# Kernel tuning notes

Hardware: AMD Instinct MI355X
Metric: run time of the kernel (lower is better)

The kernel has to match this reference:

```python
import jax, jax.numpy as jnp
import numpy as np

B, N, DIM, HID, MAXN = 2048, 65536, 256, 512, 64
MID_KEY = (MAXN + HID) // 2   # 288
MID_VAL = (DIM + HID) // 2    # 384
MID_DEC = (HID + DIM) // 2    # 384
MID_SZ  = (HID + 1) // 2      # 256

def _ln(x, g, b):
    m = x.mean(-1, keepdims=True)
    v = ((x - m) ** 2).mean(-1, keepdims=True)
    return (x - m) * jax.lax.rsqrt(v + 1e-5) * g + b

def _mish(x):
    return x * jnp.tanh(jax.nn.softplus(x))

def _mlp_ln(x, W1, b1, g, be, W2, b2):
    return _mish(_ln(x @ W1 + b1, g, be)) @ W2 + b2

def _mlp(x, W1, b1, W2, b2):
    return _mish(x @ W1 + b1) @ W2 + b2

def setup_inputs():
    key = jax.random.key(0)
    ks = iter(jax.random.split(key, 40))
    def rn(shape, s=0.05):
        return jax.random.normal(next(ks), shape, jnp.float32) * s
    x = jax.random.normal(next(ks), (N, DIM), jnp.float32)
    batch = jnp.sort(jax.random.randint(next(ks), (N,), 0, B)).astype(jnp.int32)
    z32 = lambda *s: jnp.zeros(s, jnp.float32)
    o32 = lambda *s: jnp.ones(s, jnp.float32)
    return dict(
        x=x, batch=batch, n_batches=B,
        e_rank_W=rn((DIM, 1)), e_rank_b=z32(1),
        e_card_W=rn((1, HID)), e_card_b=z32(HID),
        e_key_W1=rn((MAXN, MID_KEY)), e_key_b1=z32(MID_KEY), e_key_g=o32(MID_KEY), e_key_be=z32(MID_KEY),
        e_key_W2=rn((MID_KEY, HID)), e_key_b2=z32(HID),
        e_val_W1=rn((DIM, MID_VAL)), e_val_b1=z32(MID_VAL), e_val_g=o32(MID_VAL), e_val_be=z32(MID_VAL),
        e_val_W2=rn((MID_VAL, HID)), e_val_b2=z32(HID),
        d_key_W1=rn((MAXN, MID_KEY)), d_key_b1=z32(MID_KEY), d_key_g=o32(MID_KEY), d_key_be=z32(MID_KEY),
        d_key_W2=rn((MID_KEY, HID)), d_key_b2=z32(HID),
        d_dec_W1=rn((HID, MID_DEC)), d_dec_b1=z32(MID_DEC),
        d_dec_W2=rn((MID_DEC, DIM)), d_dec_b2=z32(DIM),
        d_size_W1=rn((HID, MID_SZ)), d_size_b1=z32(MID_SZ), d_size_g=o32(MID_SZ), d_size_be=z32(MID_SZ),
        d_size_W2=rn((MID_SZ, 1)), d_size_b2=z32(1),
    )

def reference(x, batch, n_batches, e_rank_W, e_rank_b, e_card_W, e_card_b,
              e_key_W1, e_key_b1, e_key_g, e_key_be, e_key_W2, e_key_b2,
              e_val_W1, e_val_b1, e_val_g, e_val_be, e_val_W2, e_val_b2,
              d_key_W1, d_key_b1, d_key_g, d_key_be, d_key_W2, d_key_b2,
              d_dec_W1, d_dec_b1, d_dec_W2, d_dec_b2,
              d_size_W1, d_size_b1, d_size_g, d_size_be, d_size_W2, d_size_b2):
    max_n = e_key_W1.shape[0]
    n_pts = x.shape[0]
    # ---- Encoder ----
    n = jax.ops.segment_sum(jnp.ones(n_pts, jnp.float32), batch, num_segments=n_batches).astype(jnp.int32)
    mag = jnp.abs(x @ e_rank_W + e_rank_b)[:, 0]                 # [N]
    sort_key = batch.astype(jnp.float32) * jnp.max(mag) + mag    # sort within each set by |rank|
    idx = jnp.argsort(sort_key)
    xs = x[idx]
    starts = jnp.cumsum(n) - n                                   # per-set offsets (batch is sorted)
    pos_idx = jnp.arange(n_pts) - starts[batch]                  # rank within each set
    pos = jax.nn.one_hot(pos_idx, max_n, dtype=x.dtype)
    y = _mlp_ln(xs, e_val_W1, e_val_b1, e_val_g, e_val_be, e_val_W2, e_val_b2) \
      * _mlp_ln(pos, e_key_W1, e_key_b1, e_key_g, e_key_be, e_key_W2, e_key_b2)
    z = jax.ops.segment_sum(y, batch, num_segments=n_batches) \
      + n.astype(jnp.float32)[:, None] @ e_card_W + e_card_b     # [B, HID]
    # ---- Decoder ----
    n_logits = _mlp_ln(z, d_size_W1, d_size_b1, d_size_g, d_size_be, d_size_W2, d_size_b2)  # [B, 1]
    n_dec = jnp.clip(jnp.round(n_logits[:, 0]), 0, max_n).astype(jnp.int32)
    keys = _mlp_ln(jnp.eye(max_n, dtype=x.dtype),                # onehot positions 0..max_n-1
                   d_key_W1, d_key_b1, d_key_g, d_key_be, d_key_W2, d_key_b2)  # [max_n, HID]
    zp = z[:, None, :] * keys[None, :, :]                        # [B, max_n, HID] (repeat_interleave -> dense+mask)
    xf = _mlp(zp, d_dec_W1, d_dec_b1, d_dec_W2, d_dec_b2)        # [B, max_n, DIM]
    mask = jnp.arange(max_n)[None, :] < n_dec[:, None]           # valid rows per set
    x_out = (xf * mask[..., None].astype(xf.dtype)).reshape(-1, xf.shape[-1])
    batch_out = jnp.repeat(jnp.arange(n_batches, dtype=jnp.int32), max_n)
    return x_out, batch_out, mask.reshape(-1)
```

## Files before the change

### kernel.cpp

```cpp
#include <hip/hip_runtime.h>

#define NPTS   65536
#define NB     2048
#define DIMX   256
#define HIDN   512
#define MAXNN  64
#define MIDK   288
#define MIDV   384
#define MIDD   384
#define MIDS   256

typedef unsigned short ushort_t;
typedef __attribute__((ext_vector_type(8))) short short8;
typedef __attribute__((ext_vector_type(4))) float f32x4;

__device__ __forceinline__ float mishf(float x) {
    float e = __expf(fminf(x, 30.f));
    float n = e * (e + 2.f);
    return x * n * __builtin_amdgcn_rcpf(n + 2.f);
}
__device__ __forceinline__ ushort_t f2bf(float f) {
    unsigned u = __float_as_uint(f);
    u += 0x7fffu + ((u >> 16) & 1u);
    return (ushort_t)(u >> 16);
}
__device__ __forceinline__ float bf2f(ushort_t h) {
    return __uint_as_float(((unsigned)h) << 16);
}
__device__ __forceinline__ void dma16(const void* g, void* lds) {
    __builtin_amdgcn_global_load_lds(
        (const __attribute__((address_space(1))) unsigned int*)g,
        (__attribute__((address_space(3))) unsigned int*)lds, 16, 0, 0);
}
__device__ __forceinline__ int lbound(const int* __restrict__ a, int lo, int hi, int v) {
    while (lo < hi) { int m = (lo + hi) >> 1; if (a[m] < v) lo = m + 1; else hi = m; }
    return lo;
}

#define SETUP_TBL   129
#define SETUP_Z     (SETUP_TBL + NB)
#define SETUP_WT    (SETUP_Z + 144)
#define SETUP_TOTAL (SETUP_WT + 2048)

__global__ __launch_bounds__(512)
void k_setup(const float* __restrict__ eW1, const float* __restrict__ eb1,
             const float* __restrict__ eg, const float* __restrict__ ebe,
             const float* __restrict__ eW2, const float* __restrict__ eb2,
             const float* __restrict__ dW1, const float* __restrict__ db1,
             const float* __restrict__ dg, const float* __restrict__ dbe,
             const float* __restrict__ dW2, const float* __restrict__ db2,
             float* __restrict__ enc_tbl, float* __restrict__ dec_tbl,
             const int* __restrict__ batch, const float* __restrict__ cardW,
             const float* __restrict__ cardb, float* __restrict__ z,
             const float* __restrict__ V0, ushort_t* __restrict__ T0,
             const float* __restrict__ V1, ushort_t* __restrict__ T1,
             const float* __restrict__ V2, ushort_t* __restrict__ T2,
             const float* __restrict__ V3, ushort_t* __restrict__ T3,
             const float* __restrict__ x, const float* __restrict__ rW,
             const float* __restrict__ rb, float* __restrict__ mag,
             float* __restrict__ blockmax, ushort_t* __restrict__ xb)
{
    const int blk = blockIdx.x;
    const int t = threadIdx.x;
    if (blk < SETUP_TBL) {
        const float *W1, *b1, *g, *be, *W2, *b2; float* out; int wrow;
        if (blk < 65) {
            W1 = eW1; b1 = eb1; g = eg; be = ebe; W2 = eW2; b2 = eb2;
            out = enc_tbl + blk * HIDN; wrow = (blk < 64) ? blk : -1;
        } else {
            int r = blk - 65;
            W1 = dW1; b1 = db1; g = dg; be = dbe; W2 = dW2; b2 = db2;
            out = dec_tbl + r * HIDN; wrow = r;
        }
        __shared__ float h[MIDK];
        __shared__ float red[512];
        float v = 0.f;
        if (t < MIDK) v = b1[t] + (wrow >= 0 ? W1[wrow * MIDK + t] : 0.f);
        red[t] = (t < MIDK) ? v : 0.f;
        __syncthreads();
        for (int o = 256; o > 0; o >>= 1) { if (t < o) red[t] += red[t + o]; __syncthreads(); }
        float m = red[0] / (float)MIDK;
        __syncthreads();
        float d = v - m;
        red[t] = (t < MIDK) ? d * d : 0.f;
        __syncthreads();
        for (int o = 256; o > 0; o >>= 1) { if (t < o) red[t] += red[t + o]; __syncthreads(); }
        float rs = rsqrtf(red[0] / (float)MIDK + 1e-5f);
        __syncthreads();
        if (t < MIDK) h[t] = mishf(d * rs * g[t] + be[t]);
        __syncthreads();
        float acc = b2[t];
        #pragma unroll 8
        for (int k = 0; k < MIDK; ++k) acc = fmaf(h[k], W2[k * HIDN + t], acc);
        out[t] = acc;
    } else if (blk < SETUP_Z) {
        int b = blk - SETUP_TBL;
        int s = lbound(batch, 0, NPTS, b);
        int e = lbound(batch, s, NPTS, b + 1);
        float n = (float)(e - s);
        z[b * HIDN + t] = fmaf(n, cardW[t], cardb[t]);
    } else if (blk < SETUP_WT) {
        int tile = blk - SETUP_Z;
        const float* W; ushort_t* T; int K, N;
        if (tile < 24)       { W = V0; T = T0; K = 256; N = 384; }
        else if (tile < 72)  { tile -= 24;  W = V1; T = T1; K = 384; N = 512; }
        else if (tile < 120) { tile -= 72;  W = V2; T = T2; K = 512; N = 384; }
        else                 { tile -= 120; W = V3; T = T3; K = 384; N = 256; }
        int ntn = N >> 6;
        int k0 = (tile / ntn) * 64, n0 = (tile % ntn) * 64;
        __shared__ float lds[64][65];
        #pragma unroll
        for (int pass = 0; pass < 8; ++pass) {
            int kk = pass * 8 + (t >> 6);
            lds[kk][t & 63] = W[(size_t)(k0 + kk) * N + n0 + (t & 63)];
        }
        __syncthreads();
        #pragma unroll
        for (int pass = 0; pass < 8; ++pass) {
            int nn = pass * 8 + (t >> 6);
            T[(size_t)(n0 + nn) * K + k0 + (t & 63)] = f2bf(lds[t & 63][nn]);
        }
    } else {
        int mw = blk - SETUP_WT;
        const int lane = t & 63;
        const int w = t >> 6;
        int gw = mw * 8 + w;
        float4 wv = *(const float4*)(rW + lane * 4);
        float bias = rb[0];
        float lmax = 0.f;
        for (int pt = gw; pt < NPTS; pt += 16384) {
            float4 xv = *(const float4*)(x + (size_t)pt * DIMX + lane * 4);
            ushort4 u;
            u.x = f2bf(xv.x); u.y = f2bf(xv.y); u.z = f2bf(xv.z); u.w = f2bf(xv.w);
            *(ushort4*)(xb + (size_t)pt * DIMX + lane * 4) = u;
            double d = (double)xv.x * wv.x + (double)xv.y * wv.y
                     + (double)xv.z * wv.z + (double)xv.w * wv.w;
            #pragma unroll
            for (int o = 32; o > 0; o >>= 1) d += __shfl_xor(d, o);
            float s = fabsf((float)(d + (double)bias));
            if (lane == 0) mag[pt] = s;
            lmax = fmaxf(lmax, s);
        }
        __shared__ float wm8[8];
        if (lane == 0) wm8[w] = lmax;
        __syncthreads();
        if (t == 0) {
            float m = wm8[0];
            #pragma unroll
            for (int i = 1; i < 8; ++i) m = fmaxf(m, wm8[i]);
            blockmax[mw] = m;
        }
    }
}

__global__ __launch_bounds__(256)
void k_rank(const int* __restrict__ batch, const float* __restrict__ mag,
            const float* __restrict__ blockmax, int* __restrict__ kidx)
{
    __shared__ float red[256];
    const int t = threadIdx.x;
    float m = 0.f;
    for (int i = t; i < 2048; i += 256) m = fmaxf(m, blockmax[i]);
    red[t] = m;
    __syncthreads();
    for (int o = 128; o > 0; o >>= 1) { if (t < o) red[t] = fmaxf(red[t], red[t + o]); __syncthreads(); }
    float M = red[0];

    int i = blockIdx.x * 256 + t;
    if (i >= NPTS) return;
    int b = batch[i];
    int s = lbound(batch, 0, NPTS, b);
    int e = lbound(batch, s, NPTS, b + 1);
    float kb = __fmul_rn((float)b, M);
    float ki = __fadd_rn(kb, mag[i]);
    int r = 0;
    for (int j = s; j < e; ++j) {
        float kj = __fadd_rn(kb, mag[j]);
        r += (kj < ki) || (kj == ki && j < i);
    }
    kidx[i] = (r < MAXNN) ? r : MAXNN;
}

__global__ __launch_bounds__(256)
void k_size(const float* __restrict__ z, const float* __restrict__ W1,
            const float* __restrict__ b1, const float* __restrict__ g,
            const float* __restrict__ be, const float* __restrict__ W2,
            const float* __restrict__ b2, int* __restrict__ ndec)
{
    const int b0 = blockIdx.x * 4, t = threadIdx.x;
    __shared__ float zr[4][HIDN];
    __shared__ float red[4][256];
    #pragma unroll
    for (int gI = 0; gI < 4; ++gI) {
        zr[gI][t] = z[(b0 + gI) * HIDN + t];
        zr[gI][t + 256] = z[(b0 + gI) * HIDN + 256 + t];
    }
    __syncthreads();
    float acc[4];
    float bb1 = b1[t];
    #pragma unroll
    for (int gI = 0; gI < 4; ++gI) acc[gI] = bb1;
    #pragma unroll 8
    for (int k = 0; k < HIDN; ++k) {
        float wv = W1[k * MIDS + t];
        #pragma unroll
        for (int gI = 0; gI < 4; ++gI) acc[gI] = fmaf(zr[gI][k], wv, acc[gI]);
    }
    #pragma unroll
    for (int gI = 0; gI < 4; ++gI) red[gI][t] = acc[gI];
    __syncthreads();
    for (int o = 128; o > 0; o >>= 1) {
        if (t < o) {
            #pragma unroll
            for (int gI = 0; gI < 4; ++gI) red[gI][t] += red[gI][t + o];
        }
        __syncthreads();
    }
    float mm[4];
    #pragma unroll
    for (int gI = 0; gI < 4; ++gI) mm[gI] = red[gI][0] * (1.f / 256.f);
    __syncthreads();
    #pragma unroll
    for (int gI = 0; gI < 4; ++gI) { float d = acc[gI] - mm[gI]; red[gI][t] = d * d; }
    __syncthreads();
    for (int o = 128; o > 0; o >>= 1) {
        if (t < o) {
            #pragma unroll
            for (int gI = 0; gI < 4; ++gI) red[gI][t] += red[gI][t + o];
        }
        __syncthreads();
    }
    float rs[4];
    #pragma unroll
    for (int gI = 0; gI < 4; ++gI) rs[gI] = rsqrtf(red[gI][0] * (1.f / 256.f) + 1e-5f);
    __syncthreads();
    float w2 = W2[t], gg = g[t], bbe = be[t];
    #pragma unroll
    for (int gI = 0; gI < 4; ++gI) {
        float h = mishf((acc[gI] - mm[gI]) * rs[gI] * gg + bbe);
        red[gI][t] = h * w2;
    }
    __syncthreads();
    for (int o = 128; o > 0; o >>= 1) {
        if (t < o) {
            #pragma unroll
            for (int gI = 0; gI < 4; ++gI) red[gI][t] += red[gI][t + o];
        }
        __syncthreads();
    }
    if (t < 4) {
        float logit = red[t][0] + b2[0];
        float n = rintf(logit);
        n = fminf(fmaxf(n, 0.f), 64.f);
        ndec[b0 + t] = (int)n;
    }
}

__global__ __launch_bounds__(256)
void k_post(const int* __restrict__ ndec, float* __restrict__ out_x,
            float* __restrict__ outb, float* __restrict__ outm,
            int* __restrict__ rowmap, int* __restrict__ cntpad)
{
    const int gidx = blockIdx.x * 256 + threadIdx.x;
    float4 z4 = make_float4(0.f, 0.f, 0.f, 0.f);
    float4* p = (float4*)out_x;
    #pragma unroll
    for (int i = 0; i < 32; ++i) p[gidx + i * 262144] = z4;
    if (gidx < NB * MAXNN) {
        outb[gidx] = (float)(gidx >> 6);
        outm[gidx] = ((gidx & 63) < ndec[gidx >> 6]) ? 1.f : 0.f;
    }
    if (blockIdx.x == 0) {
        __shared__ int lcnt;
        if (threadIdx.x == 0) lcnt = 0;
        __syncthreads();
        for (int b = threadIdx.x; b < NB; b += 256) {
            int n = ndec[b];
            if (n > 0) {
                int base = atomicAdd(&lcnt, n);
                for (int q = 0; q < n; ++q) rowmap[base + q] = b * 64 + q;
            }
        }
        __syncthreads();
        int c = lcnt;
        int pad = (c + 127) & ~127;
        for (int i = c + threadIdx.x; i < pad; i += 256) rowmap[i] = -1;
        if (threadIdx.x == 0) *cntpad = pad;
    }
}

__global__ __launch_bounds__(512, 2)
void k_mm_e1f(const ushort_t* __restrict__ A, const ushort_t* __restrict__ Bt,
              const float* __restrict__ bias, const float* __restrict__ g,
              const float* __restrict__ be, ushort_t* __restrict__ C)
{
    const int m0 = blockIdx.x * 128;
    __shared__ __align__(16) ushort_t As[128 * 64];
    __shared__ __align__(16) ushort_t Bs[384 * 64];
    const int t = threadIdx.x;
    const int l = t & 63;
    const int w = t >> 6;
    const int wm = (w >> 2) * 64;
    const int wq = (w & 3) * 96;
    const int l4 = (l >> 4) << 2;
    const int drow = l >> 3;
    const int dblk = (l & 7) ^ drow;

    f32x4 acc[4][6];
    #pragma unroll
    for (int a = 0; a < 4; ++a)
        #pragma unroll
        for (int b = 0; b < 6; ++b) acc[a][b] = (f32x4)0.f;

    for (int k0 = 0; k0 < DIMX; k0 += 64) {
        #pragma unroll
        for (int ii = 0; ii < 2; ++ii) {
            int i = w * 2 + ii;
            dma16(A + (size_t)(m0 + i * 8 + drow) * DIMX + k0 + dblk * 8, &As[i * 512]);
        }
        #pragma unroll
        for (int ii = 0; ii < 6; ++ii) {
            int i = w * 6 + ii;
            dma16(Bt + (size_t)(i * 8 + drow) * DIMX + k0 + dblk * 8, &Bs[i * 512]);
        }
        __syncthreads();
        #pragma unroll
        for (int ks = 0; ks < 2; ++ks) {
            int kq = ks * 4 + (l >> 4);
            short8 af[4], bfr[6];
            #pragma unroll
            for (int fm = 0; fm < 4; ++fm) {
                int row = wm + fm * 16 + (l & 15);
                af[fm] = *(const short8*)&As[row * 64 + ((kq ^ (row & 7)) << 3)];
            }
            #pragma unroll
            for (int fn = 0; fn < 6; ++fn) {
                int row = wq + fn * 16 + (l & 15);
                bfr[fn] = *(const short8*)&Bs[row * 64 + ((kq ^ (row & 7)) << 3)];
            }
            #pragma unroll
            for (int fm = 0; fm < 4; ++fm)
                #pragma unroll
                for (int fn = 0; fn < 6; ++fn)
                    acc[fm][fn] = __builtin_amdgcn_mfma_f32_16x16x32_bf16(
                        af[fm], bfr[fn], acc[fm][fn], 0, 0, 0);
        }
        __syncthreads();
    }

    float bb[6], gg[6], bee[6];
    #pragma unroll
    for (int fn = 0; fn < 6; ++fn) {
        int col = wq + fn * 16 + (l & 15);
        bb[fn] = bias[col]; gg[fn] = g[col]; bee[fn] = be[col];
    }
    #pragma unroll
    for (int fm = 0; fm < 4; ++fm)
        #pragma unroll
        for (int fn = 0; fn < 6; ++fn)
            #pragma unroll
            for (int j = 0; j < 4; ++j) acc[fm][fn][j] += bb[fn];

    float* ssum = (float*)As;
    float* ssq  = ssum + 512;
    #pragma unroll
    for (int fm = 0; fm < 4; ++fm) {
        #pragma unroll
        for (int j = 0; j < 4; ++j) {
            float s = 0.f, q = 0.f;
            #pragma unroll
            for (int fn = 0; fn < 6; ++fn) {
                float v = acc[fm][fn][j];
                s += v; q += v * v;
            }
            #pragma unroll
            for (int o = 1; o < 16; o <<= 1) {
                s += __shfl_xor(s, o);
                q += __shfl_xor(q, o);
            }
            if ((l & 15) == 0) {
                int r = wm + fm * 16 + l4 + j;
                ssum[r * 4 + (w & 3)] = s;
                ssq[r * 4 + (w & 3)] = q;
            }
        }
    }
    __syncthreads();
    #pragma unroll
    for (int fm = 0; fm < 4; ++fm) {
        #pragma unroll
        for (int j = 0; j < 4; ++j) {
            int r = wm + fm * 16 + l4 + j;
            float s = ssum[r * 4 + 0] + ssum[r * 4 + 1] + ssum[r * 4 + 2] + ssum[r * 4 + 3];
            float q = ssq[r * 4 + 0] + ssq[r * 4 + 1] + ssq[r * 4 + 2] + ssq[r * 4 + 3];
            float m = s * (1.f / 384.f);
            float var = q * (1.f / 384.f) - m * m;
            float rs = rsqrtf(var + 1e-5f);
            #pragma unroll
            for (int fn = 0; fn < 6; ++fn) {
                float v = (acc[fm][fn][j] - m) * rs * gg[fn] + bee[fn];
                C[(size_t)(m0 + r) * MIDV + wq + fn * 16 + (l & 15)] = f2bf(mishf(v));
            }
        }
    }
}

__global__ __launch_bounds__(256, 2)
void k_mm_e2(const ushort_t* __restrict__ A, const ushort_t* __restrict__ Bt,
             const float* __restrict__ bias, int K, const float* __restrict__ tbl,
             const int* __restrict__ kidx, const int* __restrict__ batch,
             float* __restrict__ zout)
{
    const int flat = blockIdx.y * gridDim.x + blockIdx.x;
    const int nx = gridDim.x;
    const int xcd = flat & 7;
    const int lin = flat >> 3;
    const int n0 = (lin % nx) * 128;
    const int m0 = ((lin / nx) + ((gridDim.y >> 3) * xcd)) * 128;
    __shared__ __align__(16) ushort_t sAB[2 * 128 * 64];
    __shared__ int barr[128];
    __shared__ int karr[128];
    ushort_t* As = sAB;
    ushort_t* Bs = sAB + 128 * 64;
    const int t = threadIdx.x;
    const int l = t & 63;
    const int w = t >> 6;
    const int wm = (w >> 1) * 64;
    const int wn = (w & 1) * 64;
    const int l4 = (l >> 4) << 2;
    const int drow = l >> 3;
    const int dblk = (l & 7) ^ drow;

    if (t < 128) { barr[t] = batch[m0 + t]; karr[t] = kidx[m0 + t]; }

    f32x4 acc[4][4];
    #pragma unroll
    for (int a = 0; a < 4; ++a)
        #pragma unroll
        for (int b = 0; b < 4; ++b) acc[a][b] = (f32x4)0.f;

    for (int k0 = 0; k0 < K; k0 += 64) {
        #pragma unroll
        for (int ii = 0; ii < 4; ++ii) {
            int i = w * 4 + ii;
            dma16(A + (size_t)(m0 + i * 8 + drow) * K + k0 + dblk * 8, &As[i * 512]);
        }
        #pragma unroll
        for (int ii = 0; ii < 4; ++ii) {
            int i = w * 4 + ii;
            dma16(Bt + (size_t)(n0 + i * 8 + drow) * K + k0 + dblk * 8, &Bs[i * 512]);
        }
        __syncthreads();
        #pragma unroll
        for (int ks = 0; ks < 2; ++ks) {
            short8 af[4], bfr[4];
            int kq = ks * 4 + (l >> 4);
            #pragma unroll
            for (int fm = 0; fm < 4; ++fm) {
                int row = wm + fm * 16 + (l & 15);
                af[fm] = *(const short8*)&As[row * 64 + ((kq ^ (row & 7)) << 3)];
            }
            #pragma unroll
            for (int fn = 0; fn < 4; ++fn) {
                int row = wn + fn * 16 + (l & 15);
                bfr[fn] = *(const short8*)&Bs[row * 64 + ((kq ^ (row & 7)) << 3)];
            }
            #pragma unroll
            for (int fm = 0; fm < 4; ++fm)
                #pragma unroll
                for (int fn = 0; fn < 4; ++fn)
                    acc[fm][fn] = __builtin_amdgcn_mfma_f32_16x16x32_bf16(
                        af[fm], bfr[fn], acc[fm][fn], 0, 0, 0);
        }
        __syncthreads();
    }

    float* yred = (float*)sAB;
    #pragma unroll
    for (int pass = 0; pass < 2; ++pass) {
        if ((w >> 1) == pass) {
            #pragma unroll
            for (int fn = 0; fn < 4; ++fn) {
                int cl = wn + fn * 16 + (l & 15);
                float bbv = bias[n0 + cl];
                #pragma unroll
                for (int fm = 0; fm < 4; ++fm) {
                    #pragma unroll
                    for (int j = 0; j < 4; ++j) {
                        int rl = fm * 16 + l4 + j;
                        float v = (acc[fm][fn][j] + bbv)
                                * tbl[karr[pass * 64 + rl] * HIDN + (n0 + cl)];
                        yred[cl * 64 + (rl ^ (cl & 31))] = v;
                    }
                }
            }
        }
        __syncthreads();
        {
            int c = t & 127, q = t >> 7;
            int gc = n0 + c;
            float run = 0.f; int curb = -1;
            #pragma unroll
            for (int ch = 0; ch < 2; ++ch) {
                float v16[16]; int b16[16];
                #pragma unroll
                for (int rr = 0; rr < 16; ++rr) {
                    int rl = q * 32 + ch * 16 + rr;
                    v16[rr] = yred[c * 64 + (rl ^ (c & 31))];
                    b16[rr] = barr[pass * 64 + rl];
                }
                #pragma unroll
                for (int rr = 0; rr < 16; ++rr) {
                    if (b16[rr] != curb) {
                        if (curb >= 0) atomicAdd(&zout[curb * HIDN + gc], run);
                        curb = b16[rr]; run = v16[rr];
                    } else run += v16[rr];
                }
            }
            atomicAdd(&zout[curb * HIDN + gc], run);
        }
        __syncthreads();
    }
}

template<int MODE>
__device__ __forceinline__
void mm_body(const ushort_t* __restrict__ A, const ushort_t* __restrict__ Bt,
             const float* __restrict__ bias, void* __restrict__ Cptr, int K,
             const float* __restrict__ tbl, const float* __restrict__ zin,
             const int* __restrict__ rowmap, const int* __restrict__ cntpad)
{
    const int flat = blockIdx.y * gridDim.x + blockIdx.x;
    const int nx = gridDim.x;
    const int xcd = flat & 7;
    const int lin = flat >> 3;
    const int n0 = (lin % nx) * 128;
    const int m0 = ((lin / nx) + ((gridDim.y >> 3) * xcd)) * 128;
    if (m0 >= *cntpad) return;
    __shared__ __align__(16) ushort_t sAB[2 * 128 * 64];
    ushort_t* As = sAB;
    ushort_t* Bs = sAB + 128 * 64;
    const int t = threadIdx.x;
    const int l = t & 63;
    const int w = t >> 6;
    const int wm = (w >> 1) * 64;
    const int wn = (w & 1) * 64;
    const int l4 = (l >> 4) << 2;
    const int drow = l >> 3;
    const int dblk = (l & 7) ^ drow;

    int g4[4], p4[4];
    if (MODE == 2) {
        #pragma unroll
        for (int ii = 0; ii < 4; ++ii) {
            int i = w * 4 + ii;
            int gr = rowmap[m0 + i * 8 + drow];
            if (gr < 0) gr = 0;
            g4[ii] = gr >> 6; p4[ii] = gr & 63;
        }
    }

    f32x4 acc[4][4];
    #pragma unroll
    for (int a = 0; a < 4; ++a)
        #pragma unroll
        for (int b = 0; b < 4; ++b) acc[a][b] = (f32x4)0.f;

    for (int k0 = 0; k0 < K; k0 += 64) {
        if (MODE == 2) {
            #pragma unroll
            for (int ii = 0; ii < 4; ++ii) {
                int i = w * 4 + ii;
                int row = i * 8 + drow;
                const float* zp = zin + g4[ii] * HIDN + k0 + dblk * 8;
                const float* kp = tbl + p4[ii] * HIDN + k0 + dblk * 8;
                float4 z0 = *(const float4*)zp;
                float4 z1 = *(const float4*)(zp + 4);
                float4 q0 = *(const float4*)kp;
                float4 q1 = *(const float4*)(kp + 4);
                ushort4 u0, u1;
                u0.x = f2bf(z0.x * q0.x); u0.y = f2bf(z0.y * q0.y);
                u0.z = f2bf(z0.z * q0.z); u0.w = f2bf(z0.w * q0.w);
                u1.x = f2bf(z1.x * q1.x); u1.y = f2bf(z1.y * q1.y);
                u1.z = f2bf(z1.z * q1.z); u1.w = f2bf(z1.w * q1.w);
                ushort_t* dst = &As[row * 64 + (l & 7) * 8];
                *(ushort4*)dst = u0;
                *(ushort4*)(dst + 4) = u1;
            }
        } else {
            #pragma unroll
            for (int ii = 0; ii < 4; ++ii) {
                int i = w * 4 + ii;
                const ushort_t* gp = A + (size_t)(m0 + i * 8 + drow) * K + k0 + dblk * 8;
                dma16(gp, &As[i * 512]);
            }
        }
        #pragma unroll
        for (int ii = 0; ii < 4; ++ii) {
            int i = w * 4 + ii;
            const ushort_t* gp = Bt + (size_t)(n0 + i * 8 + drow) * K + k0 + dblk * 8;
            dma16(gp, &Bs[i * 512]);
        }
        __syncthreads();
        #pragma unroll
        for (int ks = 0; ks < 2; ++ks) {
            short8 af[4], bfr[4];
            int kq = ks * 4 + (l >> 4);
            #pragma unroll
            for (int fm = 0; fm < 4; ++fm) {
                int row = wm + fm * 16 + (l & 15);
                af[fm] = *(const short8*)&As[row * 64 + ((kq ^ (row & 7)) << 3)];
            }
            #pragma unroll
            for (int fn = 0; fn < 4; ++fn) {
                int row = wn + fn * 16 + (l & 15);
                bfr[fn] = *(const short8*)&Bs[row * 64 + ((kq ^ (row & 7)) << 3)];
            }
            #pragma unroll
            for (int fm = 0; fm < 4; ++fm)
                #pragma unroll
                for (int fn = 0; fn < 4; ++fn)
                    acc[fm][fn] = __builtin_amdgcn_mfma_f32_16x16x32_bf16(
                        af[fm], bfr[fn], acc[fm][fn], 0, 0, 0);
        }
        __syncthreads();
    }

    if (MODE == 2) {
        ushort_t* C = (ushort_t*)Cptr;
        #pragma unroll
        for (int fm = 0; fm < 4; ++fm) {
            int gr0 = m0 + wm + fm * 16 + l4;
            #pragma unroll
            for (int fn = 0; fn < 4; ++fn) {
                int gc = n0 + wn + fn * 16 + (l & 15);
                float bbv = bias[gc];
                #pragma unroll
                for (int j = 0; j < 4; ++j)
                    C[(size_t)(gr0 + j) * MIDD + gc] = f2bf(mishf(acc[fm][fn][j] + bbv));
            }
        }
    } else {
        float* C = (float*)Cptr;
        #pragma unroll
        for (int fm = 0; fm < 4; ++fm) {
            int gr0 = m0 + wm + fm * 16 + l4;
            int om[4];
            #pragma unroll
            for (int j = 0; j < 4; ++j) om[j] = rowmap[gr0 + j];
            #pragma unroll
            for (int fn = 0; fn < 4; ++fn) {
                int gc = n0 + wn + fn * 16 + (l & 15);
                float bbv = bias[gc];
                #pragma unroll
                for (int j = 0; j < 4; ++j)
                    if (om[j] >= 0) C[(size_t)om[j] * DIMX + gc] = acc[fm][fn][j] + bbv;
            }
        }
    }
}

__global__ __launch_bounds__(256, 2)
void k_mm_d1(const ushort_t* Bt, const float* bias, void* C, int K,
             const float* tbl, const float* zin, const int* rowmap, const int* cntpad)
{ mm_body<2>(nullptr, Bt, bias, C, K, tbl, zin, rowmap, cntpad); }

__global__ __launch_bounds__(256, 2)
void k_mm_d2(const ushort_t* A, const ushort_t* Bt, const float* bias, void* C, int K,
             const int* rowmap, const int* cntpad)
{ mm_body<3>(A, Bt, bias, C, K, nullptr, nullptr, rowmap, cntpad); }

extern "C" void kernel_launch(void* const* d_in, const int* in_sizes, int n_in,
                              void* d_out, int out_size, void* d_ws, size_t ws_size,
                              hipStream_t stream)
{
    const float* x        = (const float*)d_in[0];
    const int*   batch    = (const int*)  d_in[1];
    const float* e_rank_W = (const float*)d_in[3];
    const float* e_rank_b = (const float*)d_in[4];
    const float* e_card_W = (const float*)d_in[5];
    const float* e_card_b = (const float*)d_in[6];
    const float* e_key_W1 = (const float*)d_in[7];
    const float* e_key_b1 = (const float*)d_in[8];
    const float* e_key_g  = (const float*)d_in[9];
    const float* e_key_be = (const float*)d_in[10];
    const float* e_key_W2 = (const float*)d_in[11];
    const float* e_key_b2 = (const float*)d_in[12];
    const float* e_val_W1 = (const float*)d_in[13];
    const float* e_val_b1 = (const float*)d_in[14];
    const float* e_val_g  = (const float*)d_in[15];
    const float* e_val_be = (const float*)d_in[16];
    const float* e_val_W2 = (const float*)d_in[17];
    const float* e_val_b2 = (const float*)d_in[18];
    const float* d_key_W1 = (const float*)d_in[19];
    const float* d_key_b1 = (const float*)d_in[20];
    const float* d_key_g  = (const float*)d_in[21];
    const float* d_key_be = (const float*)d_in[22];
    const float* d_key_W2 = (const float*)d_in[23];
    const float* d_key_b2 = (const float*)d_in[24];
    const float* d_dec_W1 = (const float*)d_in[25];
    const float* d_dec_b1 = (const float*)d_in[26];
    const float* d_dec_W2 = (const float*)d_in[27];
    const float* d_dec_b2 = (const float*)d_in[28];
    const float* d_size_W1= (const float*)d_in[29];
    const float* d_size_b1= (const float*)d_in[30];
    const float* d_size_g = (const float*)d_in[31];
    const float* d_size_be= (const float*)d_in[32];
    const float* d_size_W2= (const float*)d_in[33];
    const float* d_size_b2= (const float*)d_in[34];

    char* ws = (char*)d_ws;
    float*        blockmax= (float*)       (ws + 0);
    int*          kidx    = (int*)         (ws + 8704);
    float*        mag     = (float*)       (ws + 270848);
    float*        enc_tbl = (float*)       (ws + 532992);
    float*        dec_tbl = (float*)       (ws + 666112);
    float*        z       = (float*)       (ws + 797184);
    int*          ndec    = (int*)         (ws + 4991488);
    int*          cntpad  = (int*)         (ws + 4999684);
    int*          rowmap  = (int*)         (ws + 5000192);
    ushort_t*     evW1t   = (ushort_t*)    (ws + 5524480);
    ushort_t*     evW2t   = (ushort_t*)    (ws + 5721088);
    ushort_t*     ddW1t   = (ushort_t*)    (ws + 6114304);
    ushort_t*     ddW2t   = (ushort_t*)    (ws + 6507520);
    ushort_t*     xb      = (ushort_t*)    (ws + 6704384);
    ushort_t*     Hb      = (ushort_t*)    (ws + 6704384 + 33554432);
    ushort_t*     Hd      = (ushort_t*)    (ws + 6704384 + 33554432);

    float* out_x = (float*)d_out;
    float* out_b = out_x + (size_t)NB * MAXNN * DIMX;
    float* out_m = out_b + NB * MAXNN;

    k_setup<<<dim3(SETUP_TOTAL), dim3(512), 0, stream>>>(
        e_key_W1, e_key_b1, e_key_g, e_key_be, e_key_W2, e_key_b2,
        d_key_W1, d_key_b1, d_key_g, d_key_be, d_key_W2, d_key_b2,
        enc_tbl, dec_tbl, batch, e_card_W, e_card_b, z,
        e_val_W1, evW1t, e_val_W2, evW2t, d_dec_W1, ddW1t, d_dec_W2, ddW2t,
        x, e_rank_W, e_rank_b, mag, blockmax, xb);
    k_rank<<<dim3(256), dim3(256), 0, stream>>>(batch, mag, blockmax, kidx);

    k_mm_e1f<<<dim3(512), dim3(512), 0, stream>>>(xb, evW1t, e_val_b1,
                                                  e_val_g, e_val_be, Hb);
    k_mm_e2<<<dim3(4, 512), dim3(256), 0, stream>>>(Hb, evW2t, e_val_b2, MIDV,
                                                    enc_tbl, kidx, batch, z);

    k_size<<<dim3(NB / 4), dim3(256), 0, stream>>>(z, d_size_W1, d_size_b1, d_size_g,
                                                   d_size_be, d_size_W2, d_size_b2, ndec);
    k_post<<<dim3(1024), dim3(256), 0, stream>>>(ndec, out_x, out_b, out_m,
                                                 rowmap, cntpad);
    k_mm_d1<<<dim3(3, 1024), dim3(256), 0, stream>>>(ddW1t, d_dec_b1, Hd, HIDN,
                                                     dec_tbl, z, rowmap, cntpad);
    k_mm_d2<<<dim3(2, 1024), dim3(256), 0, stream>>>(Hd, ddW2t, d_dec_b2, out_x, MIDD,
                                                     rowmap, cntpad);
}
```

Before: 449.7 us.

## Fold rank kernel into e1f grid and move output zeroing into setup

The per-point rank computation is merged into the first encoder GEMM kernel as extra blocks, which removes one launch and lets ranking overlap with the matmul blocks. Zeroing of the 128 MB output buffer moves from k_post into extra setup blocks, so it runs alongside the other independent setup work instead of on the critical path after k_size. Launch bounds for three GEMM kernels rise from 2 to 3 blocks per CU, which may force register spills. The rank blocks still depend on blockmax written by k_setup, and that ordering holds because they run in a later launch.

Measured after the change: 454.0 us. Within noise of the previous version (+1.0%).

```diff
diff --git a/kernel.cpp b/kernel.cpp
--- a/kernel.cpp
+++ b/kernel.cpp
@@ -40,7 +40,8 @@
 #define SETUP_TBL   129
 #define SETUP_Z     (SETUP_TBL + NB)
 #define SETUP_WT    (SETUP_Z + 144)
-#define SETUP_TOTAL (SETUP_WT + 2048)
+#define SETUP_MAG   (SETUP_WT + 2048)
+#define SETUP_TOTAL (SETUP_MAG + 2048)
 
 __global__ __launch_bounds__(512)
 void k_setup(const float* __restrict__ eW1, const float* __restrict__ eb1,
@@ -58,7 +59,8 @@
              const float* __restrict__ V3, ushort_t* __restrict__ T3,
              const float* __restrict__ x, const float* __restrict__ rW,
              const float* __restrict__ rb, float* __restrict__ mag,
-             float* __restrict__ blockmax, ushort_t* __restrict__ xb)
+             float* __restrict__ blockmax, ushort_t* __restrict__ xb,
+             float* __restrict__ out_x)
 {
     const int blk = blockIdx.x;
     const int t = threadIdx.x;
@@ -120,7 +122,7 @@
             int nn = pass * 8 + (t >> 6);
             T[(size_t)(n0 + nn) * K + k0 + (t & 63)] = f2bf(lds[t & 63][nn]);
         }
-    } else {
+    } else if (blk < SETUP_MAG) {
         int mw = blk - SETUP_WT;
         const int lane = t & 63;
         const int w = t >> 6;
@@ -150,35 +152,159 @@
             for (int i = 1; i < 8; ++i) m = fmaxf(m, wm8[i]);
             blockmax[mw] = m;
         }
-    }
-}
-
-__global__ __launch_bounds__(256)
-void k_rank(const int* __restrict__ batch, const float* __restrict__ mag,
-            const float* __restrict__ blockmax, int* __restrict__ kidx)
+    } else {
+        int zb = blk - SETUP_MAG;
+        float4 z4 = make_float4(0.f, 0.f, 0.f, 0.f);
+        float4* p = (float4*)out_x;
+        int base = zb * 512 + t;
+        #pragma unroll
+        for (int i = 0; i < 8; ++i) p[base + i * 1048576] = z4;
+    }
+}
+
+__global__ __launch_bounds__(512, 2)
+void k_mm_e1f(const ushort_t* __restrict__ A, const ushort_t* __restrict__ Bt,
+              const float* __restrict__ bias, const float* __restrict__ g,
+              const float* __restrict__ be, ushort_t* __restrict__ C,
+              const int* __restrict__ batch, const float* __restrict__ mag,
+              const float* __restrict__ blockmax, int* __restrict__ kidx)
 {
-    __shared__ float red[256];
+    __shared__ __align__(16) ushort_t As[128 * 64];
+    __shared__ __align__(16) ushort_t Bs[384 * 64];
     const int t = threadIdx.x;
-    float m = 0.f;
-    for (int i = t; i < 2048; i += 256) m = fmaxf(m, blockmax[i]);
-    red[t] = m;
+
+    if (blockIdx.x >= 512) {
+        float* red = (float*)As;
+        float m = 0.f;
+        for (int i = t; i < 2048; i += 512) m = fmaxf(m, blockmax[i]);
+        red[t] = m;
+        __syncthreads();
+        for (int o = 256; o > 0; o >>= 1) {
+            if (t < o) red[t] = fmaxf(red[t], red[t + o]);
+            __syncthreads();
+        }
+        float M = red[0];
+        int i = (blockIdx.x - 512) * 512 + t;
+        int b = batch[i];
+        int s = lbound(batch, 0, NPTS, b);
+        int e = lbound(batch, s, NPTS, b + 1);
+        float kb = __fmul_rn((float)b, M);
+        float ki = __fadd_rn(kb, mag[i]);
+        int r = 0;
+        for (int j = s; j < e; ++j) {
+            float kj = __fadd_rn(kb, mag[j]);
+            r += (kj < ki) || (kj == ki && j < i);
+        }
+        kidx[i] = (r < MAXNN) ? r : MAXNN;
+        return;
+    }
+
+    const int m0 = blockIdx.x * 128;
+    const int l = t & 63;
+    const int w = t >> 6;
+    const int wm = (w >> 2) * 64;
+    const int wq = (w & 3) * 96;
+    const int l4 = (l >> 4) << 2;
+    const int drow = l >> 3;
+    const int dblk = (l & 7) ^ drow;
+
+    f32x4 acc[4][6];
+    #pragma unroll
+    for (int a = 0; a < 4; ++a)
+        #pragma unroll
+        for (int b = 0; b < 6; ++b) acc[a][b] = (f32x4)0.f;
+
+    for (int k0 = 0; k0 < DIMX; k0 += 64) {
+        #pragma unroll
+        for (int ii = 0; ii < 2; ++ii) {
+            int i = w * 2 + ii;
+            dma16(A + (size_t)(m0 + i * 8 + drow) * DIMX + k0 + dblk * 8, &As[i * 512]);
+        }
+        #pragma unroll
+        for (int ii = 0; ii < 6; ++ii) {
+            int i = w * 6 + ii;
+            dma16(Bt + (size_t)(i * 8 + drow) * DIMX + k0 + dblk * 8, &Bs[i * 512]);
+        }
+        __syncthreads();
+        #pragma unroll
+        for (int ks = 0; ks < 2; ++ks) {
+            int kq = ks * 4 + (l >> 4);
+            short8 af[4], bfr[6];
+            #pragma unroll
+            for (int fm = 0; fm < 4; ++fm) {
+                int row = wm + fm * 16 + (l & 15);
+                af[fm] = *(const short8*)&As[row * 64 + ((kq ^ (row & 7)) << 3)];
+            }
+            #pragma unroll
+            for (int fn = 0; fn < 6; ++fn) {
+                int row = wq + fn * 16 + (l & 15);
+                bfr[fn] = *(const short8*)&Bs[row * 64 + ((kq ^ (row & 7)) << 3)];
+            }
+            #pragma unroll
+            for (int fm = 0; fm < 4; ++fm)
+                #pragma unroll
+                for (int fn = 0; fn < 6; ++fn)
+                    acc[fm][fn] = __builtin_amdgcn_mfma_f32_16x16x32_bf16(
+                        af[fm], bfr[fn], acc[fm][fn], 0, 0, 0);
+        }
+        __syncthreads();
+    }
+
+    float bb[6], gg[6], bee[6];
+    #pragma unroll
+    for (int fn = 0; fn < 6; ++fn) {
+        int col = wq + fn * 16 + (l & 15);
+        bb[fn] = bias[col]; gg[fn] = g[col]; bee[fn] = be[col];
+    }
+    #pragma unroll
+    for (int fm = 0; fm < 4; ++fm)
+        #pragma unroll
+        for (int fn = 0; fn < 6; ++fn)
+            #pragma unroll
+            for (int j = 0; j < 4; ++j) acc[fm][fn][j] += bb[fn];
+
+    float* ssum = (float*)As;
+    float* ssq  = ssum + 512;
+    #pragma unroll
+    for (int fm = 0; fm < 4; ++fm) {
+        #pragma unroll
+        for (int j = 0; j < 4; ++j) {
+            float s = 0.f, q = 0.f;
+            #pragma unroll
+            for (int fn = 0; fn < 6; ++fn) {
+                float v = acc[fm][fn][j];
+                s += v; q += v * v;
+            }
+            #pragma unroll
+            for (int o = 1; o < 16; o <<= 1) {
+                s += __shfl_xor(s, o);
+                q += __shfl_xor(q, o);
+            }
+            if ((l & 15) == 0) {
+                int r = wm + fm * 16 + l4 + j;
+                ssum[r * 4 + (w & 3)] = s;
+                ssq[r * 4 + (w & 3)] = q;
+            }
+        }
+    }
     __syncthreads();
-    for (int o = 128; o > 0; o >>= 1) { if (t < o) red[t] = fmaxf(red[t], red[t + o]); __syncthreads(); }
-    float M = red[0];
-
-    int i = blockIdx.x * 256 + t;
-    if (i >= NPTS) return;
-    int b = batch[i];
-    int s = lbound(batch, 0, NPTS, b);
-    int e = lbound(batch, s, NPTS, b + 1);
-    float kb = __fmul_rn((float)b, M);
-    float ki = __fadd_rn(kb, mag[i]);
-    int r = 0;
-    for (int j = s; j < e; ++j) {
-        float kj = __fadd_rn(kb, mag[j]);
-        r += (kj < ki) || (kj == ki && j < i);
-    }
-    kidx[i] = (r < MAXNN) ? r : MAXNN;
+    #pragma unroll
+    for (int fm = 0; fm < 4; ++fm) {
+        #pragma unroll
+        for (int j = 0; j < 4; ++j) {
+            int r = wm + fm * 16 + l4 + j;
+            float s = ssum[r * 4 + 0] + ssum[r * 4 + 1] + ssum[r * 4 + 2] + ssum[r * 4 + 3];
+            float q = ssq[r * 4 + 0] + ssq[r * 4 + 1] + ssq[r * 4 + 2] + ssq[r * 4 + 3];
+            float m = s * (1.f / 384.f);
+            float var = q * (1.f / 384.f) - m * m;
+            float rs = rsqrtf(var + 1e-5f);
+            #pragma unroll
+            for (int fn = 0; fn < 6; ++fn) {
+                float v = (acc[fm][fn][j] - m) * rs * gg[fn] + bee[fn];
+                C[(size_t)(m0 + r) * MIDV + wq + fn * 16 + (l & 15)] = f2bf(mishf(v));
+            }
+        }
+    }
 }
 
 __global__ __launch_bounds__(256)
@@ -257,19 +383,13 @@
 }
 
 __global__ __launch_bounds__(256)
-void k_post(const int* __restrict__ ndec, float* __restrict__ out_x,
-            float* __restrict__ outb, float* __restrict__ outm,
-            int* __restrict__ rowmap, int* __restrict__ cntpad)
+void k_post(const int* __restrict__ ndec, float* __restrict__ outb,
+            float* __restrict__ outm, int* __restrict__ rowmap,
+            int* __restrict__ cntpad)
 {
     const int gidx = blockIdx.x * 256 + threadIdx.x;
-    float4 z4 = make_float4(0.f, 0.f, 0.f, 0.f);
-    float4* p = (float4*)out_x;
-    #pragma unroll
-    for (int i = 0; i < 32; ++i) p[gidx + i * 262144] = z4;
-    if (gidx < NB * MAXNN) {
-        outb[gidx] = (float)(gidx >> 6);
-        outm[gidx] = ((gidx & 63) < ndec[gidx >> 6]) ? 1.f : 0.f;
-    }
+    outb[gidx] = (float)(gidx >> 6);
+    outm[gidx] = ((gidx & 63) < ndec[gidx >> 6]) ? 1.f : 0.f;
     if (blockIdx.x == 0) {
         __shared__ int lcnt;
         if (threadIdx.x == 0) lcnt = 0;
@@ -289,123 +409,7 @@
     }
 }
 
-__global__ __launch_bounds__(512, 2)
-void k_mm_e1f(const ushort_t* __restrict__ A, const ushort_t* __restrict__ Bt,
-              const float* __restrict__ bias, const float* __restrict__ g,
-              const float* __restrict__ be, ushort_t* __restrict__ C)
-{
-    const int m0 = blockIdx.x * 128;
-    __shared__ __align__(16) ushort_t As[128 * 64];
-    __shared__ __align__(16) ushort_t Bs[384 * 64];
-    const int t = threadIdx.x;
-    const int l = t & 63;
-    const int w = t >> 6;
-    const int wm = (w >> 2) * 64;
-    const int wq = (w & 3) * 96;
-    const int l4 = (l >> 4) << 2;
-    const int drow = l >> 3;
-    const int dblk = (l & 7) ^ drow;
-
-    f32x4 acc[4][6];
-    #pragma unroll
-    for (int a = 0; a < 4; ++a)
-        #pragma unroll
-        for (int b = 0; b < 6; ++b) acc[a][b] = (f32x4)0.f;
-
-    for (int k0 = 0; k0 < DIMX; k0 += 64) {
-        #pragma unroll
-        for (int ii = 0; ii < 2; ++ii) {
-            int i = w * 2 + ii;
-            dma16(A + (size_t)(m0 + i * 8 + drow) * DIMX + k0 + dblk * 8, &As[i * 512]);
-        }
-        #pragma unroll
-        for (int ii = 0; ii < 6; ++ii) {
-            int i = w * 6 + ii;
-            dma16(Bt + (size_t)(i * 8 + drow) * DIMX + k0 + dblk * 8, &Bs[i * 512]);
-        }
-        __syncthreads();
-        #pragma unroll
-        for (int ks = 0; ks < 2; ++ks) {
-            int kq = ks * 4 + (l >> 4);
-            short8 af[4], bfr[6];
-            #pragma unroll
-            for (int fm = 0; fm < 4; ++fm) {
-                int row = wm + fm * 16 + (l & 15);
-                af[fm] = *(const short8*)&As[row * 64 + ((kq ^ (row & 7)) << 3)];
-            }
-            #pragma unroll
-            for (int fn = 0; fn < 6; ++fn) {
-                int row = wq + fn * 16 + (l & 15);
-                bfr[fn] = *(const short8*)&Bs[row * 64 + ((kq ^ (row & 7)) << 3)];
-            }
-            #pragma unroll
-            for (int fm = 0; fm < 4; ++fm)
-                #pragma unroll
-                for (int fn = 0; fn < 6; ++fn)
-                    acc[fm][fn] = __builtin_amdgcn_mfma_f32_16x16x32_bf16(
-                        af[fm], bfr[fn], acc[fm][fn], 0, 0, 0);
-        }
-        __syncthreads();
-    }
-
-    float bb[6], gg[6], bee[6];
-    #pragma unroll
-    for (int fn = 0; fn < 6; ++fn) {
-        int col = wq + fn * 16 + (l & 15);
-        bb[fn] = bias[col]; gg[fn] = g[col]; bee[fn] = be[col];
-    }
-    #pragma unroll
-    for (int fm = 0; fm < 4; ++fm)
-        #pragma unroll
-        for (int fn = 0; fn < 6; ++fn)
-            #pragma unroll
-            for (int j = 0; j < 4; ++j) acc[fm][fn][j] += bb[fn];
-
-    float* ssum = (float*)As;
-    float* ssq  = ssum + 512;
-    #pragma unroll
-    for (int fm = 0; fm < 4; ++fm) {
-        #pragma unroll
-        for (int j = 0; j < 4; ++j) {
-            float s = 0.f, q = 0.f;
-            #pragma unroll
-            for (int fn = 0; fn < 6; ++fn) {
-                float v = acc[fm][fn][j];
-                s += v; q += v * v;
-            }
-            #pragma unroll
-            for (int o = 1; o < 16; o <<= 1) {
-                s += __shfl_xor(s, o);
-                q += __shfl_xor(q, o);
-            }
-            if ((l & 15) == 0) {
-                int r = wm + fm * 16 + l4 + j;
-                ssum[r * 4 + (w & 3)] = s;
-                ssq[r * 4 + (w & 3)] = q;
-            }
-        }
-    }
-    __syncthreads();
-    #pragma unroll
-    for (int fm = 0; fm < 4; ++fm) {
-        #pragma unroll
-        for (int j = 0; j < 4; ++j) {
-            int r = wm + fm * 16 + l4 + j;
-            float s = ssum[r * 4 + 0] + ssum[r * 4 + 1] + ssum[r * 4 + 2] + ssum[r * 4 + 3];
-            float q = ssq[r * 4 + 0] + ssq[r * 4 + 1] + ssq[r * 4 + 2] + ssq[r * 4 + 3];
-            float m = s * (1.f / 384.f);
-            float var = q * (1.f / 384.f) - m * m;
-            float rs = rsqrtf(var + 1e-5f);
-            #pragma unroll
-            for (int fn = 0; fn < 6; ++fn) {
-                float v = (acc[fm][fn][j] - m) * rs * gg[fn] + bee[fn];
-                C[(size_t)(m0 + r) * MIDV + wq + fn * 16 + (l & 15)] = f2bf(mishf(v));
-            }
-        }
-    }
-}
-
-__global__ __launch_bounds__(256, 2)
+__global__ __launch_bounds__(256, 3)
 void k_mm_e2(const ushort_t* __restrict__ A, const ushort_t* __restrict__ Bt,
              const float* __restrict__ bias, int K, const float* __restrict__ tbl,
              const int* __restrict__ kidx, const int* __restrict__ batch,
@@ -660,12 +664,12 @@
     }
 }
 
-__global__ __launch_bounds__(256, 2)
+__global__ __launch_bounds__(256, 3)
 void k_mm_d1(const ushort_t* Bt, const float* bias, void* C, int K,
              const float* tbl, const float* zin, const int* rowmap, const int* cntpad)
 { mm_body<2>(nullptr, Bt, bias, C, K, tbl, zin, rowmap, cntpad); }
 
-__global__ __launch_bounds__(256, 2)
+__global__ __launch_bounds__(256, 3)
 void k_mm_d2(const ushort_t* A, const ushort_t* Bt, const float* bias, void* C, int K,
              const int* rowmap, const int* cntpad)
 { mm_body<3>(A, Bt, bias, C, K, nullptr, nullptr, rowmap, cntpad); }
@@ -736,18 +740,17 @@
         d_key_W1, d_key_b1, d_key_g, d_key_be, d_key_W2, d_key_b2,
         enc_tbl, dec_tbl, batch, e_card_W, e_card_b, z,
         e_val_W1, evW1t, e_val_W2, evW2t, d_dec_W1, ddW1t, d_dec_W2, ddW2t,
-        x, e_rank_W, e_rank_b, mag, blockmax, xb);
-    k_rank<<<dim3(256), dim3(256), 0, stream>>>(batch, mag, blockmax, kidx);
-
-    k_mm_e1f<<<dim3(512), dim3(512), 0, stream>>>(xb, evW1t, e_val_b1,
-                                                  e_val_g, e_val_be, Hb);
+        x, e_rank_W, e_rank_b, mag, blockmax, xb, out_x);
+
+    k_mm_e1f<<<dim3(640), dim3(512), 0, stream>>>(xb, evW1t, e_val_b1,
+                                                  e_val_g, e_val_be, Hb,
+                                                  batch, mag, blockmax, kidx);
     k_mm_e2<<<dim3(4, 512), dim3(256), 0, stream>>>(Hb, evW2t, e_val_b2, MIDV,
                                                     enc_tbl, kidx, batch, z);
 
     k_size<<<dim3(NB / 4), dim3(256), 0, stream>>>(z, d_size_W1, d_size_b1, d_size_g,
                                                    d_size_be, d_size_W2, d_size_b2, ndec);
-    k_post<<<dim3(1024), dim3(256), 0, stream>>>(ndec, out_x, out_b, out_m,
-                                                 rowmap, cntpad);
+    k_post<<<dim3(512), dim3(256), 0, stream>>>(ndec, out_b, out_m, rowmap, cntpad);
     k_mm_d1<<<dim3(3, 1024), dim3(256), 0, stream>>>(ddW1t, d_dec_b1, Hd, HIDN,
                                                      dec_tbl, z, rowmap, cntpad);
     k_mm_d2<<<dim3(2, 1024), dim3(256), 0, stream>>>(Hd, ddW2t, d_dec_b2, out_x, MIDD,
```
